# Kernel optimization log

Measured on AMD Instinct MI355X. Metric: run time of the kernel, lower is better.

Reference implementation:

```python
import jax, jax.numpy as jnp
import numpy as np
import math

D_MODEL = 512
NUM_HEADS = 8
D_K = D_MODEL // NUM_HEADS
MAX_LEN = 500
BATCH = 32
SEQ = 480


def setup_inputs() -> dict:
    key = jax.random.key(0)
    ks = jax.random.split(key, 10)
    s = 0.02
    x = jax.random.normal(ks[0], (BATCH, SEQ, D_MODEL), dtype=jnp.float32)
    wq = jax.random.normal(ks[1], (D_MODEL, D_MODEL), dtype=jnp.float32) * s
    bq = jnp.zeros((D_MODEL,), jnp.float32)
    wk = jax.random.normal(ks[2], (D_MODEL, D_MODEL), dtype=jnp.float32) * s
    bk = jnp.zeros((D_MODEL,), jnp.float32)
    wv = jax.random.normal(ks[3], (D_MODEL, D_MODEL), dtype=jnp.float32) * s
    bv = jnp.zeros((D_MODEL,), jnp.float32)
    wo = jax.random.normal(ks[4], (D_MODEL, D_MODEL), dtype=jnp.float32) * s
    bo = jnp.zeros((D_MODEL,), jnp.float32)
    rel_bias = jax.random.normal(ks[5], (NUM_HEADS, MAX_LEN, MAX_LEN), dtype=jnp.float32) * 0.02
    return {"x": x, "wq": wq, "bq": bq, "wk": wk, "bk": bk, "wv": wv,
            "bv": bv, "wo": wo, "bo": bo, "rel_bias": rel_bias}


def reference(x, wq, bq, wk, bk, wv, bv, wo, bo, rel_bias):
    B, S, D = x.shape
    H, dk = NUM_HEADS, D_K
    scale = math.sqrt(dk)
    # QKV projections -> [B, H, S, dk]
    q = (x @ wq + bq).reshape(B, S, H, dk).transpose(0, 2, 1, 3)
    k = (x @ wk + bk).reshape(B, S, H, dk).transpose(0, 2, 1, 3)
    v = (x @ wv + bv).reshape(B, S, H, dk).transpose(0, 2, 1, 3)
    scores = jnp.einsum('bhqd,bhkd->bhqk', q, k) / scale
    scores = scores + rel_bias[None, :, :S, :S]
    causal = jnp.triu(jnp.ones((S, S), dtype=bool), k=1)  # True where j > i
    scores = jnp.where(causal[None, None], -jnp.inf, scores)
    attn = jax.nn.softmax(scores, axis=-1)
    ctx = jnp.einsum('bhqk,bhkd->bhqd', attn, v)
    ctx = ctx.transpose(0, 2, 1, 3).reshape(B, S, D)
    out = ctx @ wo + bo
    return out, attn.mean(axis=1)
```

## Files before the change

kernel.cpp:

```cpp
#include <hip/hip_runtime.h>
#include <hip/hip_bf16.h>


typedef unsigned short ushort_t;
typedef __attribute__((ext_vector_type(8))) short short8;
typedef __attribute__((ext_vector_type(4))) float floatx4;

#define NB 32
#define NS 480
#define ND 512
#define NH 8
#define NDK 64
#define MAXLEN 500
#define KSTRIDE 72
#define BSTRIDE 68

__device__ __forceinline__ ushort_t f2bf(float f) {
  union { float f; unsigned u; } v; v.f = f;
  unsigned r = v.u + 0x7FFFu + ((v.u >> 16) & 1u);
  return (ushort_t)(r >> 16);
}

#define GLOAD_LDS16(g, l)                                                      \
  __builtin_amdgcn_global_load_lds(                                            \
      (const __attribute__((address_space(1))) void*)(g),                      \
      (__attribute__((address_space(3))) void*)(l), 16, 0, 0)

__global__ void cvt_x(const float* __restrict__ x, ushort_t* __restrict__ xb) {
  int idx = blockIdx.x * 256 + threadIdx.x;
  float4 v = ((const float4*)x)[idx];
  ushort4 o;
  o.x = f2bf(v.x); o.y = f2bf(v.y); o.z = f2bf(v.z); o.w = f2bf(v.w);
  ((ushort4*)xb)[idx] = o;
}

__global__ void cvt_w(const float* __restrict__ wq, const float* __restrict__ wk,
                      const float* __restrict__ wv, const float* __restrict__ wo,
                      ushort_t* __restrict__ wqT, ushort_t* __restrict__ wkT,
                      ushort_t* __restrict__ wvT, ushort_t* __restrict__ woT) {
  __shared__ float t[32][33];
  int z = blockIdx.z;
  const float* w = (z == 0) ? wq : (z == 1) ? wk : (z == 2) ? wv : wo;
  ushort_t* wT = (z == 0) ? wqT : (z == 1) ? wkT : (z == 2) ? wvT : woT;
  int k0 = blockIdx.x * 32, n0 = blockIdx.y * 32;
  int tx = threadIdx.x & 31, ty = threadIdx.x >> 5;
#pragma unroll
  for (int yy = 0; yy < 4; ++yy)
    t[ty + yy * 8][tx] = w[(k0 + ty + yy * 8) * ND + n0 + tx];
  __syncthreads();
#pragma unroll
  for (int yy = 0; yy < 4; ++yy)
    wT[(n0 + ty + yy * 8) * ND + k0 + tx] = f2bf(t[tx][ty + yy * 8]);
}

__global__ __launch_bounds__(256)
void qkv_gemm(const ushort_t* __restrict__ xb,
              const ushort_t* __restrict__ wqT, const ushort_t* __restrict__ wkT,
              const ushort_t* __restrict__ wvT,
              const float* __restrict__ bq, const float* __restrict__ bk,
              const float* __restrict__ bv,
              ushort_t* __restrict__ qb, ushort_t* __restrict__ kb,
              ushort_t* __restrict__ vT) {
  __shared__ __align__(16) ushort_t sA[128 * 32];
  __shared__ __align__(16) ushort_t sB[128 * 32];
  const int tid = threadIdx.x;
  const int wid = tid >> 6, lane = tid & 63;
  const int lm = lane & 15, quad = lane >> 4;
  const int wr = wid >> 1, wc = wid & 1;
  const int row0 = blockIdx.x * 128;
  const int col0 = blockIdx.y * 128;
  const int z = blockIdx.z;
  const ushort_t* Bt = (z == 0) ? wqT : (z == 1) ? wkT : wvT;
  const float* bias = (z == 0) ? bq : (z == 1) ? bk : bv;

  floatx4 zero4 = {0.f, 0.f, 0.f, 0.f};
  floatx4 acc[4][4];
#pragma unroll
  for (int i = 0; i < 4; ++i)
#pragma unroll
    for (int j = 0; j < 4; ++j) acc[i][j] = zero4;

  for (int k0 = 0; k0 < ND; k0 += 32) {
#pragma unroll
    for (int c = 0; c < 2; ++c) {
      int li = c * 256 + tid;
      int row = li >> 2, kc = li & 3;
      GLOAD_LDS16(xb + (row0 + row) * ND + k0 + kc * 8, sA + (c * 256 + wid * 64) * 8);
      GLOAD_LDS16(Bt + (col0 + row) * ND + k0 + kc * 8, sB + (c * 256 + wid * 64) * 8);
    }
    __syncthreads();
    short8 a[4], b[4];
#pragma unroll
    for (int i = 0; i < 4; ++i)
      a[i] = *(const short8*)&sA[(wr * 64 + i * 16 + lm) * 32 + quad * 8];
#pragma unroll
    for (int j = 0; j < 4; ++j)
      b[j] = *(const short8*)&sB[(wc * 64 + j * 16 + lm) * 32 + quad * 8];
#pragma unroll
    for (int i = 0; i < 4; ++i)
#pragma unroll
      for (int j = 0; j < 4; ++j)
        acc[i][j] = __builtin_amdgcn_mfma_f32_16x16x32_bf16(a[i], b[j], acc[i][j], 0, 0, 0);
    __syncthreads();
  }

  float bsv[4];
#pragma unroll
  for (int j = 0; j < 4; ++j) bsv[j] = bias[col0 + wc * 64 + j * 16 + lm];

#pragma unroll
  for (int i = 0; i < 4; ++i)
#pragma unroll
    for (int j = 0; j < 4; ++j)
#pragma unroll
      for (int r = 0; r < 4; ++r) {
        int m = row0 + wr * 64 + i * 16 + quad * 4 + r;
        int n = col0 + wc * 64 + j * 16 + lm;
        float val = acc[i][j][r] + bsv[j];
        int bb = m / NS, s = m - bb * NS;
        int h = n >> 6, d = n & 63;
        ushort_t o = f2bf(val);
        if (z == 0)      qb[((bb * NH + h) * NS + s) * NDK + d] = o;
        else if (z == 1) kb[((bb * NH + h) * NS + s) * NDK + d] = o;
        else             vT[((bb * NH + h) * NDK + d) * NS + s] = o;
      }
}

__global__ __launch_bounds__(256)
void flash_attn(const ushort_t* __restrict__ qb, const ushort_t* __restrict__ kb,
                const ushort_t* __restrict__ vT, const float* __restrict__ rel_bias,
                ushort_t* __restrict__ ctxb, float* __restrict__ cst) {
  const int bh = blockIdx.x;
  const int b = bh >> 3, h = bh & 7;
  const int qt = 7 - blockIdx.y;
  const int tid = threadIdx.x;
  const int wid = tid >> 6, lane = tid & 63;
  const int lm = lane & 15, quad = lane >> 4;

  __shared__ __align__(16) ushort_t sP[4][16 * 32];

  const int q0w = qt * 64 + wid * 16;
  if (q0w >= NS) return;

  const ushort_t* qh = qb + (size_t)bh * NS * NDK;
  const ushort_t* kh = kb + (size_t)bh * NS * NDK;
  const ushort_t* vh = vT + (size_t)bh * NDK * NS;

  short8 aq0 = *(const short8*)&qh[(q0w + lm) * NDK + quad * 8];
  short8 aq1 = *(const short8*)&qh[(q0w + lm) * NDK + 32 + quad * 8];

  float lsum[4];
  floatx4 O[4];
  floatx4 zero4 = {0.f, 0.f, 0.f, 0.f};
#pragma unroll
  for (int r = 0; r < 4; ++r) lsum[r] = 0.f;
#pragma unroll
  for (int jd = 0; jd < 4; ++jd) O[jd] = zero4;

  const int qmax = q0w + 15;
  const int nkt = qmax / 32 + 1;
  const int irow = q0w + quad * 4;

  for (int kt = 0; kt < nkt; ++kt) {
    const int kv0 = kt * 32 + 2 * lm;
    short8 bk00 = *(const short8*)&kh[kv0 * NDK + quad * 8];
    short8 bk01 = *(const short8*)&kh[kv0 * NDK + 32 + quad * 8];
    short8 bk10 = *(const short8*)&kh[(kv0 + 1) * NDK + quad * 8];
    short8 bk11 = *(const short8*)&kh[(kv0 + 1) * NDK + 32 + quad * 8];
    short8 bv[4];
#pragma unroll
    for (int jd = 0; jd < 4; ++jd)
      bv[jd] = *(const short8*)&vh[(jd * 16 + lm) * NS + kt * 32 + quad * 8];

    floatx4 s0 = zero4, s1 = zero4;
    s0 = __builtin_amdgcn_mfma_f32_16x16x32_bf16(aq0, bk00, s0, 0, 0, 0);
    s0 = __builtin_amdgcn_mfma_f32_16x16x32_bf16(aq1, bk01, s0, 0, 0, 0);
    s1 = __builtin_amdgcn_mfma_f32_16x16x32_bf16(aq0, bk10, s1, 0, 0, 0);
    s1 = __builtin_amdgcn_mfma_f32_16x16x32_bf16(aq1, bk11, s1, 0, 0, 0);

#pragma unroll
    for (int r = 0; r < 4; ++r) {
      int i = irow + r;
      float2 bb = *(const float2*)&rel_bias[((size_t)h * MAXLEN + i) * MAXLEN + kv0];
      float v0 = s0[r] * 0.125f + bb.x;
      float v1 = s1[r] * 0.125f + bb.y;
      if (kv0 > i) v0 = -1e30f;
      if (kv0 + 1 > i) v1 = -1e30f;
      float p0 = __expf(v0);
      float p1 = __expf(v1);
      lsum[r] += p0 + p1;
      unsigned packed = (unsigned)f2bf(p0) | ((unsigned)f2bf(p1) << 16);
      *(unsigned*)&sP[wid][(quad * 4 + r) * 32 + 2 * lm] = packed;
    }

    short8 ap = *(const short8*)&sP[wid][lm * 32 + quad * 8];
#pragma unroll
    for (int jd = 0; jd < 4; ++jd)
      O[jd] = __builtin_amdgcn_mfma_f32_16x16x32_bf16(ap, bv[jd], O[jd], 0, 0, 0);
  }

#pragma unroll
  for (int off = 1; off < 16; off <<= 1)
#pragma unroll
    for (int r = 0; r < 4; ++r) lsum[r] += __shfl_xor(lsum[r], off, 64);

  float rinv[4];
#pragma unroll
  for (int r = 0; r < 4; ++r) rinv[r] = 1.f / lsum[r];
#pragma unroll
  for (int jd = 0; jd < 4; ++jd)
#pragma unroll
    for (int r = 0; r < 4; ++r)
      ctxb[((size_t)b * NS + irow + r) * ND + h * NDK + jd * 16 + lm] =
          f2bf(O[jd][r] * rinv[r]);
  if (lm == 0) {
#pragma unroll
    for (int r = 0; r < 4; ++r)
      cst[((size_t)bh * 0 + (size_t)b * NS + irow + r) * NH + h] = __logf(lsum[r]);
  }
}

__global__ __launch_bounds__(256)
void attn_mean_k(const ushort_t* __restrict__ qb, const ushort_t* __restrict__ kb,
                 const float* __restrict__ rel_bias, const float* __restrict__ cst,
                 float* __restrict__ attn_mean) {
  const int b = blockIdx.x;
  const int tile = blockIdx.y;
  const int it = tile >> 3, jt = tile & 7;
  const int tid = threadIdx.x;

  if (jt > it) {
    int r = tid >> 2;
    int i = it * 64 + r;
    if (i < NS) {
      float4 z = {0.f, 0.f, 0.f, 0.f};
#pragma unroll
      for (int cc = 0; cc < 4; ++cc) {
        int j = jt * 64 + (tid & 3) * 16 + cc * 4;
        if (j < NS) *(float4*)&attn_mean[((size_t)b * NS + i) * NS + j] = z;
      }
    }
    return;
  }

  __shared__ __align__(16) ushort_t sK[2][64 * KSTRIDE];
  __shared__ __align__(16) float sB[2][64 * BSTRIDE];

  const int wid = tid >> 6, lane = tid & 63;
  const int lm = lane & 15, quad = lane >> 4;
  const int i0 = it * 64 + wid * 16;
  const bool active = (i0 < NS);
  const int j0t = jt * 64;

  float cstv[4][8];
#pragma unroll
  for (int r = 0; r < 4; ++r) {
    int i = min(i0 + quad * 4 + r, NS - 1);
    float4 c0 = *(const float4*)&cst[((size_t)b * NS + i) * NH];
    float4 c1 = *(const float4*)&cst[((size_t)b * NS + i) * NH + 4];
    cstv[r][0] = c0.x; cstv[r][1] = c0.y; cstv[r][2] = c0.z; cstv[r][3] = c0.w;
    cstv[r][4] = c1.x; cstv[r][5] = c1.y; cstv[r][6] = c1.z; cstv[r][7] = c1.w;
  }

  const int krow0 = tid >> 3, koff = (tid & 7) * 8;
  const int brow0 = tid >> 4, boff = (tid & 15) * 4;
  const int kr0 = min(j0t + krow0, NS - 1);
  const int kr1 = min(j0t + krow0 + 32, NS - 1);

  uint4 kreg[2];
  float4 breg[4];
  short8 qa0, qa1, qn0, qn1;

  {
    const ushort_t* kh = kb + (size_t)(b * NH) * NS * NDK;
    kreg[0] = *(const uint4*)&kh[kr0 * NDK + koff];
    kreg[1] = *(const uint4*)&kh[kr1 * NDK + koff];
#pragma unroll
    for (int c = 0; c < 4; ++c) {
      int ri = min(it * 64 + brow0 + c * 16, NS - 1);
      breg[c] = *(const float4*)&rel_bias[((size_t)0 * MAXLEN + ri) * MAXLEN + j0t + boff];
    }
    const ushort_t* qh = qb + (size_t)(b * NH) * NS * NDK;
    int qi = min(i0 + lm, NS - 1);
    qa0 = *(const short8*)&qh[qi * NDK + quad * 8];
    qa1 = *(const short8*)&qh[qi * NDK + 32 + quad * 8];
    *(uint4*)&sK[0][krow0 * KSTRIDE + koff] = kreg[0];
    *(uint4*)&sK[0][(krow0 + 32) * KSTRIDE + koff] = kreg[1];
#pragma unroll
    for (int c = 0; c < 4; ++c)
      *(float4*)&sB[0][(brow0 + c * 16) * BSTRIDE + boff] = breg[c];
  }
  __syncthreads();

  floatx4 zero4 = {0.f, 0.f, 0.f, 0.f};
  floatx4 acc[4];
#pragma unroll
  for (int jj = 0; jj < 4; ++jj) acc[jj] = zero4;

#pragma unroll
  for (int h = 0; h < NH; ++h) {
    const int buf = h & 1;
    if (h < NH - 1) {
      const ushort_t* kh = kb + (size_t)(b * NH + h + 1) * NS * NDK;
      kreg[0] = *(const uint4*)&kh[kr0 * NDK + koff];
      kreg[1] = *(const uint4*)&kh[kr1 * NDK + koff];
#pragma unroll
      for (int c = 0; c < 4; ++c) {
        int ri = min(it * 64 + brow0 + c * 16, NS - 1);
        breg[c] = *(const float4*)&rel_bias[((size_t)(h + 1) * MAXLEN + ri) * MAXLEN +
                                            j0t + boff];
      }
      const ushort_t* qh = qb + (size_t)(b * NH + h + 1) * NS * NDK;
      int qi = min(i0 + lm, NS - 1);
      qn0 = *(const short8*)&qh[qi * NDK + quad * 8];
      qn1 = *(const short8*)&qh[qi * NDK + 32 + quad * 8];
    }

#pragma unroll
    for (int jj = 0; jj < 4; ++jj) {
      short8 bk0 = *(const short8*)&sK[buf][(jj * 16 + lm) * KSTRIDE + quad * 8];
      short8 bk1 = *(const short8*)&sK[buf][(jj * 16 + lm) * KSTRIDE + 32 + quad * 8];
      floatx4 s = zero4;
      s = __builtin_amdgcn_mfma_f32_16x16x32_bf16(qa0, bk0, s, 0, 0, 0);
      s = __builtin_amdgcn_mfma_f32_16x16x32_bf16(qa1, bk1, s, 0, 0, 0);
#pragma unroll
      for (int r = 0; r < 4; ++r) {
        float bias = sB[buf][(quad * 4 + r) * BSTRIDE + jj * 16 + lm];
        float p = __expf(s[r] * 0.125f + bias - cstv[r][h]);
        int i = i0 + quad * 4 + r;
        int j = j0t + jj * 16 + lm;
        if (j > i) p = 0.f;
        acc[jj][r] += p;
      }
    }

    if (h < NH - 1) {
      *(uint4*)&sK[buf ^ 1][krow0 * KSTRIDE + koff] = kreg[0];
      *(uint4*)&sK[buf ^ 1][(krow0 + 32) * KSTRIDE + koff] = kreg[1];
#pragma unroll
      for (int c = 0; c < 4; ++c)
        *(float4*)&sB[buf ^ 1][(brow0 + c * 16) * BSTRIDE + boff] = breg[c];
      qa0 = qn0; qa1 = qn1;
    }
    __syncthreads();
  }

  if (active) {
#pragma unroll
    for (int jj = 0; jj < 4; ++jj) {
      int j = j0t + jj * 16 + lm;
      if (j < NS) {
#pragma unroll
        for (int r = 0; r < 4; ++r)
          attn_mean[((size_t)b * NS + i0 + quad * 4 + r) * NS + j] =
              acc[jj][r] * 0.125f;
      }
    }
  }
}

__global__ __launch_bounds__(256)
void out_gemm(const ushort_t* __restrict__ ctxb, const ushort_t* __restrict__ woT,
              const float* __restrict__ bo, float* __restrict__ out) {
  __shared__ __align__(16) ushort_t sA[128 * 32];
  __shared__ __align__(16) ushort_t sB[128 * 32];
  const int tid = threadIdx.x;
  const int wid = tid >> 6, lane = tid & 63;
  const int lm = lane & 15, quad = lane >> 4;
  const int wr = wid >> 1, wc = wid & 1;
  const int row0 = blockIdx.x * 128;
  const int col0 = blockIdx.y * 128;

  floatx4 zero4 = {0.f, 0.f, 0.f, 0.f};
  floatx4 acc[4][4];
#pragma unroll
  for (int i = 0; i < 4; ++i)
#pragma unroll
    for (int j = 0; j < 4; ++j) acc[i][j] = zero4;

  for (int k0 = 0; k0 < ND; k0 += 32) {
#pragma unroll
    for (int c = 0; c < 2; ++c) {
      int li = c * 256 + tid;
      int row = li >> 2, kc = li & 3;
      GLOAD_LDS16(ctxb + (row0 + row) * ND + k0 + kc * 8, sA + (c * 256 + wid * 64) * 8);
      GLOAD_LDS16(woT + (col0 + row) * ND + k0 + kc * 8, sB + (c * 256 + wid * 64) * 8);
    }
    __syncthreads();
    short8 a[4], b[4];
#pragma unroll
    for (int i = 0; i < 4; ++i)
      a[i] = *(const short8*)&sA[(wr * 64 + i * 16 + lm) * 32 + quad * 8];
#pragma unroll
    for (int j = 0; j < 4; ++j)
      b[j] = *(const short8*)&sB[(wc * 64 + j * 16 + lm) * 32 + quad * 8];
#pragma unroll
    for (int i = 0; i < 4; ++i)
#pragma unroll
      for (int j = 0; j < 4; ++j)
        acc[i][j] = __builtin_amdgcn_mfma_f32_16x16x32_bf16(a[i], b[j], acc[i][j], 0, 0, 0);
    __syncthreads();
  }

  float bsv[4];
#pragma unroll
  for (int j = 0; j < 4; ++j) bsv[j] = bo[col0 + wc * 64 + j * 16 + lm];

#pragma unroll
  for (int i = 0; i < 4; ++i)
#pragma unroll
    for (int j = 0; j < 4; ++j)
#pragma unroll
      for (int r = 0; r < 4; ++r) {
        int m = row0 + wr * 64 + i * 16 + quad * 4 + r;
        int n = col0 + wc * 64 + j * 16 + lm;
        out[m * ND + n] = acc[i][j][r] + bsv[j];
      }
}

extern "C" void kernel_launch(void* const* d_in, const int* in_sizes, int n_in,
                              void* d_out, int out_size, void* d_ws, size_t ws_size,
                              hipStream_t stream) {
  const float* x  = (const float*)d_in[0];
  const float* wq = (const float*)d_in[1];
  const float* bq = (const float*)d_in[2];
  const float* wk = (const float*)d_in[3];
  const float* bk = (const float*)d_in[4];
  const float* wv = (const float*)d_in[5];
  const float* bv = (const float*)d_in[6];
  const float* wo = (const float*)d_in[7];
  const float* bo = (const float*)d_in[8];
  const float* rel_bias = (const float*)d_in[9];

  char* w = (char*)d_ws;
  ushort_t* xb  = (ushort_t*)w;
  ushort_t* wqT = (ushort_t*)(w + 15728640);
  ushort_t* wkT = wqT + 262144;
  ushort_t* wvT = wkT + 262144;
  ushort_t* woT = wvT + 262144;
  ushort_t* qb  = (ushort_t*)(w + 15728640 + 4 * 524288);
  ushort_t* kb  = qb + 7864320;
  ushort_t* vTb = kb + 7864320;
  ushort_t* ctxb = vTb + 7864320;
  float* cstat = (float*)w;

  float* out0 = (float*)d_out;
  float* attn_mean = out0 + 7864320;

  cvt_x<<<dim3(7680), dim3(256), 0, stream>>>(x, xb);
  cvt_w<<<dim3(16, 16, 4), dim3(256), 0, stream>>>(wq, wk, wv, wo, wqT, wkT, wvT, woT);
  qkv_gemm<<<dim3(120, 4, 3), dim3(256), 0, stream>>>(xb, wqT, wkT, wvT, bq, bk, bv,
                                                      qb, kb, vTb);
  flash_attn<<<dim3(256, 8), dim3(256), 0, stream>>>(qb, kb, vTb, rel_bias, ctxb,
                                                     cstat);
  attn_mean_k<<<dim3(32, 64), dim3(256), 0, stream>>>(qb, kb, rel_bias, cstat,
                                                      attn_mean);
  out_gemm<<<dim3(120, 4), dim3(256), 0, stream>>>(ctxb, woT, bo, out0);
}
```

Before: 270.6 us.

## Split V projection into transposed GEMM and use swizzled 64-wide K tiles

Moves the V projection into its own GEMM that computes W_v^T · x^T per batch, so the transposed V output is written with contiguous stores instead of the strided scattered stores of the old epilogue. All projection GEMMs now load 64-wide K tiles into LDS with an XOR swizzle, which halves the number of barriers per K loop and is meant to avoid LDS bank conflicts. The cstat buffer moves to a separate workspace region so it no longer aliases xb, which the new separate V GEMM still reads. The costs are an extra kernel launch, doubled LDS use per block, and clamped padded rows in the 480-length dimension of the V GEMM.

```diff
diff --git a/kernel.cpp b/kernel.cpp
--- a/kernel.cpp
+++ b/kernel.cpp
@@ -54,15 +54,12 @@
 }
 
 __global__ __launch_bounds__(256)
-void qkv_gemm(const ushort_t* __restrict__ xb,
-              const ushort_t* __restrict__ wqT, const ushort_t* __restrict__ wkT,
-              const ushort_t* __restrict__ wvT,
-              const float* __restrict__ bq, const float* __restrict__ bk,
-              const float* __restrict__ bv,
-              ushort_t* __restrict__ qb, ushort_t* __restrict__ kb,
-              ushort_t* __restrict__ vT) {
-  __shared__ __align__(16) ushort_t sA[128 * 32];
-  __shared__ __align__(16) ushort_t sB[128 * 32];
+void qk_gemm(const ushort_t* __restrict__ xb,
+             const ushort_t* __restrict__ wqT, const ushort_t* __restrict__ wkT,
+             const float* __restrict__ bq, const float* __restrict__ bk,
+             ushort_t* __restrict__ qb, ushort_t* __restrict__ kb) {
+  __shared__ __align__(16) ushort_t sA[128 * 64];
+  __shared__ __align__(16) ushort_t sB[128 * 64];
   const int tid = threadIdx.x;
   const int wid = tid >> 6, lane = tid & 63;
   const int lm = lane & 15, quad = lane >> 4;
@@ -70,8 +67,8 @@
   const int row0 = blockIdx.x * 128;
   const int col0 = blockIdx.y * 128;
   const int z = blockIdx.z;
-  const ushort_t* Bt = (z == 0) ? wqT : (z == 1) ? wkT : wvT;
-  const float* bias = (z == 0) ? bq : (z == 1) ? bk : bv;
+  const ushort_t* Bt = (z == 0) ? wqT : wkT;
+  const float* bias = (z == 0) ? bq : bk;
 
   floatx4 zero4 = {0.f, 0.f, 0.f, 0.f};
   floatx4 acc[4][4];
@@ -80,27 +77,35 @@
 #pragma unroll
     for (int j = 0; j < 4; ++j) acc[i][j] = zero4;
 
-  for (int k0 = 0; k0 < ND; k0 += 32) {
-#pragma unroll
-    for (int c = 0; c < 2; ++c) {
+  for (int k0 = 0; k0 < ND; k0 += 64) {
+#pragma unroll
+    for (int c = 0; c < 4; ++c) {
       int li = c * 256 + tid;
-      int row = li >> 2, kc = li & 3;
-      GLOAD_LDS16(xb + (row0 + row) * ND + k0 + kc * 8, sA + (c * 256 + wid * 64) * 8);
-      GLOAD_LDS16(Bt + (col0 + row) * ND + k0 + kc * 8, sB + (c * 256 + wid * 64) * 8);
-    }
-    __syncthreads();
-    short8 a[4], b[4];
-#pragma unroll
-    for (int i = 0; i < 4; ++i)
-      a[i] = *(const short8*)&sA[(wr * 64 + i * 16 + lm) * 32 + quad * 8];
-#pragma unroll
-    for (int j = 0; j < 4; ++j)
-      b[j] = *(const short8*)&sB[(wc * 64 + j * 16 + lm) * 32 + quad * 8];
-#pragma unroll
-    for (int i = 0; i < 4; ++i)
-#pragma unroll
-      for (int j = 0; j < 4; ++j)
-        acc[i][j] = __builtin_amdgcn_mfma_f32_16x16x32_bf16(a[i], b[j], acc[i][j], 0, 0, 0);
+      int row = li >> 3, kc = li & 7;
+      int kcs = kc ^ (row & 7);
+      GLOAD_LDS16(xb + (row0 + row) * ND + k0 + kcs * 8, sA + (c * 256 + wid * 64) * 8);
+      GLOAD_LDS16(Bt + (col0 + row) * ND + k0 + kcs * 8, sB + (c * 256 + wid * 64) * 8);
+    }
+    __syncthreads();
+#pragma unroll
+    for (int h2 = 0; h2 < 2; ++h2) {
+      short8 a[4], b[4];
+#pragma unroll
+      for (int i = 0; i < 4; ++i) {
+        int row = wr * 64 + i * 16 + lm;
+        a[i] = *(const short8*)&sA[row * 64 + (((h2 << 2) | quad) ^ (lm & 7)) * 8];
+      }
+#pragma unroll
+      for (int j = 0; j < 4; ++j) {
+        int row = wc * 64 + j * 16 + lm;
+        b[j] = *(const short8*)&sB[row * 64 + (((h2 << 2) | quad) ^ (lm & 7)) * 8];
+      }
+#pragma unroll
+      for (int i = 0; i < 4; ++i)
+#pragma unroll
+        for (int j = 0; j < 4; ++j)
+          acc[i][j] = __builtin_amdgcn_mfma_f32_16x16x32_bf16(a[i], b[j], acc[i][j], 0, 0, 0);
+    }
     __syncthreads();
   }
 
@@ -120,10 +125,78 @@
         int bb = m / NS, s = m - bb * NS;
         int h = n >> 6, d = n & 63;
         ushort_t o = f2bf(val);
-        if (z == 0)      qb[((bb * NH + h) * NS + s) * NDK + d] = o;
-        else if (z == 1) kb[((bb * NH + h) * NS + s) * NDK + d] = o;
-        else             vT[((bb * NH + h) * NDK + d) * NS + s] = o;
-      }
+        if (z == 0) qb[((bb * NH + h) * NS + s) * NDK + d] = o;
+        else        kb[((bb * NH + h) * NS + s) * NDK + d] = o;
+      }
+}
+
+__global__ __launch_bounds__(256)
+void v_gemm(const ushort_t* __restrict__ xb, const ushort_t* __restrict__ wvT,
+            const float* __restrict__ bv, ushort_t* __restrict__ vT) {
+  __shared__ __align__(16) ushort_t sA[128 * 64];
+  __shared__ __align__(16) ushort_t sB[128 * 64];
+  const int tid = threadIdx.x;
+  const int wid = tid >> 6, lane = tid & 63;
+  const int lm = lane & 15, quad = lane >> 4;
+  const int wr = wid >> 1, wc = wid & 1;
+  const int row0 = blockIdx.x * 128;
+  const int col0 = blockIdx.y * 128;
+  const int b = blockIdx.z;
+  const ushort_t* xbb = xb + (size_t)b * NS * ND;
+
+  floatx4 zero4 = {0.f, 0.f, 0.f, 0.f};
+  floatx4 acc[4][4];
+#pragma unroll
+  for (int i = 0; i < 4; ++i)
+#pragma unroll
+    for (int j = 0; j < 4; ++j) acc[i][j] = zero4;
+
+  for (int k0 = 0; k0 < ND; k0 += 64) {
+#pragma unroll
+    for (int c = 0; c < 4; ++c) {
+      int li = c * 256 + tid;
+      int row = li >> 3, kc = li & 7;
+      int kcs = kc ^ (row & 7);
+      GLOAD_LDS16(wvT + (row0 + row) * ND + k0 + kcs * 8, sA + (c * 256 + wid * 64) * 8);
+      int srow = min(col0 + row, NS - 1);
+      GLOAD_LDS16(xbb + srow * ND + k0 + kcs * 8, sB + (c * 256 + wid * 64) * 8);
+    }
+    __syncthreads();
+#pragma unroll
+    for (int h2 = 0; h2 < 2; ++h2) {
+      short8 a[4], b2[4];
+#pragma unroll
+      for (int i = 0; i < 4; ++i) {
+        int row = wr * 64 + i * 16 + lm;
+        a[i] = *(const short8*)&sA[row * 64 + (((h2 << 2) | quad) ^ (lm & 7)) * 8];
+      }
+#pragma unroll
+      for (int j = 0; j < 4; ++j) {
+        int row = wc * 64 + j * 16 + lm;
+        b2[j] = *(const short8*)&sB[row * 64 + (((h2 << 2) | quad) ^ (lm & 7)) * 8];
+      }
+#pragma unroll
+      for (int i = 0; i < 4; ++i)
+#pragma unroll
+        for (int j = 0; j < 4; ++j)
+          acc[i][j] = __builtin_amdgcn_mfma_f32_16x16x32_bf16(a[i], b2[j], acc[i][j], 0, 0, 0);
+    }
+    __syncthreads();
+  }
+
+#pragma unroll
+  for (int i = 0; i < 4; ++i)
+#pragma unroll
+    for (int r = 0; r < 4; ++r) {
+      int m = row0 + wr * 64 + i * 16 + quad * 4 + r;
+      float bias = bv[m];
+#pragma unroll
+      for (int j = 0; j < 4; ++j) {
+        int n = col0 + wc * 64 + j * 16 + lm;
+        if (n < NS)
+          vT[((size_t)b * 512 + m) * NS + n] = f2bf(acc[i][j][r] + bias);
+      }
+    }
 }
 
 __global__ __launch_bounds__(256)
@@ -167,10 +240,10 @@
     short8 bk01 = *(const short8*)&kh[kv0 * NDK + 32 + quad * 8];
     short8 bk10 = *(const short8*)&kh[(kv0 + 1) * NDK + quad * 8];
     short8 bk11 = *(const short8*)&kh[(kv0 + 1) * NDK + 32 + quad * 8];
-    short8 bv[4];
+    short8 bv2[4];
 #pragma unroll
     for (int jd = 0; jd < 4; ++jd)
-      bv[jd] = *(const short8*)&vh[(jd * 16 + lm) * NS + kt * 32 + quad * 8];
+      bv2[jd] = *(const short8*)&vh[(jd * 16 + lm) * NS + kt * 32 + quad * 8];
 
     floatx4 s0 = zero4, s1 = zero4;
     s0 = __builtin_amdgcn_mfma_f32_16x16x32_bf16(aq0, bk00, s0, 0, 0, 0);
@@ -196,7 +269,7 @@
     short8 ap = *(const short8*)&sP[wid][lm * 32 + quad * 8];
 #pragma unroll
     for (int jd = 0; jd < 4; ++jd)
-      O[jd] = __builtin_amdgcn_mfma_f32_16x16x32_bf16(ap, bv[jd], O[jd], 0, 0, 0);
+      O[jd] = __builtin_amdgcn_mfma_f32_16x16x32_bf16(ap, bv2[jd], O[jd], 0, 0, 0);
   }
 
 #pragma unroll
@@ -216,7 +289,7 @@
   if (lm == 0) {
 #pragma unroll
     for (int r = 0; r < 4; ++r)
-      cst[((size_t)bh * 0 + (size_t)b * NS + irow + r) * NH + h] = __logf(lsum[r]);
+      cst[((size_t)b * NS + irow + r) * NH + h] = __logf(lsum[r]);
   }
 }
 
@@ -362,8 +435,8 @@
 __global__ __launch_bounds__(256)
 void out_gemm(const ushort_t* __restrict__ ctxb, const ushort_t* __restrict__ woT,
               const float* __restrict__ bo, float* __restrict__ out) {
-  __shared__ __align__(16) ushort_t sA[128 * 32];
-  __shared__ __align__(16) ushort_t sB[128 * 32];
+  __shared__ __align__(16) ushort_t sA[128 * 64];
+  __shared__ __align__(16) ushort_t sB[128 * 64];
   const int tid = threadIdx.x;
   const int wid = tid >> 6, lane = tid & 63;
   const int lm = lane & 15, quad = lane >> 4;
@@ -378,27 +451,35 @@
 #pragma unroll
     for (int j = 0; j < 4; ++j) acc[i][j] = zero4;
 
-  for (int k0 = 0; k0 < ND; k0 += 32) {
-#pragma unroll
-    for (int c = 0; c < 2; ++c) {
+  for (int k0 = 0; k0 < ND; k0 += 64) {
+#pragma unroll
+    for (int c = 0; c < 4; ++c) {
       int li = c * 256 + tid;
-      int row = li >> 2, kc = li & 3;
-      GLOAD_LDS16(ctxb + (row0 + row) * ND + k0 + kc * 8, sA + (c * 256 + wid * 64) * 8);
-      GLOAD_LDS16(woT + (col0 + row) * ND + k0 + kc * 8, sB + (c * 256 + wid * 64) * 8);
-    }
-    __syncthreads();
-    short8 a[4], b[4];
-#pragma unroll
-    for (int i = 0; i < 4; ++i)
-      a[i] = *(const short8*)&sA[(wr * 64 + i * 16 + lm) * 32 + quad * 8];
-#pragma unroll
-    for (int j = 0; j < 4; ++j)
-      b[j] = *(const short8*)&sB[(wc * 64 + j * 16 + lm) * 32 + quad * 8];
-#pragma unroll
-    for (int i = 0; i < 4; ++i)
-#pragma unroll
-      for (int j = 0; j < 4; ++j)
-        acc[i][j] = __builtin_amdgcn_mfma_f32_16x16x32_bf16(a[i], b[j], acc[i][j], 0, 0, 0);
+      int row = li >> 3, kc = li & 7;
+      int kcs = kc ^ (row & 7);
+      GLOAD_LDS16(ctxb + (row0 + row) * ND + k0 + kcs * 8, sA + (c * 256 + wid * 64) * 8);
+      GLOAD_LDS16(woT + (col0 + row) * ND + k0 + kcs * 8, sB + (c * 256 + wid * 64) * 8);
+    }
+    __syncthreads();
+#pragma unroll
+    for (int h2 = 0; h2 < 2; ++h2) {
+      short8 a[4], b[4];
+#pragma unroll
+      for (int i = 0; i < 4; ++i) {
+        int row = wr * 64 + i * 16 + lm;
+        a[i] = *(const short8*)&sA[row * 64 + (((h2 << 2) | quad) ^ (lm & 7)) * 8];
+      }
+#pragma unroll
+      for (int j = 0; j < 4; ++j) {
+        int row = wc * 64 + j * 16 + lm;
+        b[j] = *(const short8*)&sB[row * 64 + (((h2 << 2) | quad) ^ (lm & 7)) * 8];
+      }
+#pragma unroll
+      for (int i = 0; i < 4; ++i)
+#pragma unroll
+        for (int j = 0; j < 4; ++j)
+          acc[i][j] = __builtin_amdgcn_mfma_f32_16x16x32_bf16(a[i], b[j], acc[i][j], 0, 0, 0);
+    }
     __syncthreads();
   }
 
@@ -442,15 +523,15 @@
   ushort_t* kb  = qb + 7864320;
   ushort_t* vTb = kb + 7864320;
   ushort_t* ctxb = vTb + 7864320;
-  float* cstat = (float*)w;
+  float* cstat = (float*)(w + 15728640 + 4 * 524288 + 4 * 15728640);
 
   float* out0 = (float*)d_out;
   float* attn_mean = out0 + 7864320;
 
   cvt_x<<<dim3(7680), dim3(256), 0, stream>>>(x, xb);
   cvt_w<<<dim3(16, 16, 4), dim3(256), 0, stream>>>(wq, wk, wv, wo, wqT, wkT, wvT, woT);
-  qkv_gemm<<<dim3(120, 4, 3), dim3(256), 0, stream>>>(xb, wqT, wkT, wvT, bq, bk, bv,
-                                                      qb, kb, vTb);
+  qk_gemm<<<dim3(120, 4, 2), dim3(256), 0, stream>>>(xb, wqT, wkT, bq, bk, qb, kb);
+  v_gemm<<<dim3(4, 4, 32), dim3(256), 0, stream>>>(xb, wvT, bv, vTb);
   flash_attn<<<dim3(256, 8), dim3(256), 0, stream>>>(qb, kb, vTb, rel_bias, ctxb,
                                                      cstat);
   attn_mean_k<<<dim3(32, 64), dim3(256), 0, stream>>>(qb, kb, rel_bias, cstat,
```

Result: faster. 261.8 us (-3.2%).
